# Optimization experiments

Hardware: AMD Instinct MI355X
Metric: run time of the kernel (lower is better)

Reference implementation:

```python
import jax, jax.numpy as jnp
import numpy as np
from jax import lax

N = 40       # num_users
K = 20       # num_channels
F = 3        # num_features (conv length dim)
SS = K * N   # state_size = 800
B = 16384


def _conv1d(x, w, b):
    # x: [B, C_in, L], w: [C_out, C_in, 3], SAME padding (pad=1)
    y = lax.conv_general_dilated(x, w, window_strides=(1,), padding=[(1, 1)],
                                 dimension_numbers=('NCH', 'OIH', 'NCH'))
    return y + b[None, :, None]


def _get_mask(state):
    # state: [B, SS, F]; status feature is index 2 (== -1 since F=3)
    visited = state[:, :, 2] != 0.0                      # [B, SS]
    vm = visited.reshape(B, K, N)                        # [B, K, N] (flat idx = chan*N + user)
    user_any = vm.any(axis=1)                            # [B, N]: user visited on any channel
    chan_full = vm.sum(axis=2) >= 2                      # [B, K]: channel has >=2 users
    mask = visited \
        | jnp.broadcast_to(user_any[:, None, :], (B, K, N)).reshape(B, SS) \
        | jnp.broadcast_to(chan_full[:, :, None], (B, K, N)).reshape(B, SS)
    return mask


def setup_inputs() -> dict:
    key = jax.random.key(0)
    ks = jax.random.split(key, 12)
    state = jax.random.normal(ks[0], (B, SS, F), jnp.float32)
    keep = jax.random.bernoulli(ks[1], 0.02, (B, SS)).astype(jnp.float32)
    state = state.at[:, :, 2].multiply(keep)
    s = 0.02
    w1 = jax.random.normal(ks[2], (128, SS, 3), jnp.float32) * s
    b1 = jnp.zeros((128,), jnp.float32)
    w2 = jax.random.normal(ks[3], (256, 128, 3), jnp.float32) * s
    b2 = jnp.zeros((256,), jnp.float32)
    w3 = jax.random.normal(ks[4], (128, 256, 3), jnp.float32) * s
    b3 = jnp.zeros((128,), jnp.float32)
    wl1 = jax.random.normal(ks[5], (64 * F, 128 * F), jnp.float32) * s   # [192, 384]
    bl1 = jnp.zeros((64 * F,), jnp.float32)
    wl2 = jax.random.normal(ks[6], (SS, 64 * F), jnp.float32) * s        # [800, 192]
    bl2 = jnp.zeros((SS,), jnp.float32)
    return {"state": state, "w1": w1, "b1": b1, "w2": w2, "b2": b2,
            "w3": w3, "b3": b3, "wl1": wl1, "bl1": bl1, "wl2": wl2, "bl2": bl2}


def reference(state, w1, b1, w2, b2, w3, b3, wl1, bl1, wl2, bl2):
    mask = _get_mask(state)
    x = jax.nn.relu(_conv1d(state, w1, b1))   # [B,128,3]
    x = jax.nn.relu(_conv1d(x, w2, b2))       # [B,256,3]
    x = jax.nn.relu(_conv1d(x, w3, b3))       # [B,128,3]
    x = x.reshape(B, -1)                      # [B,384]
    x = jax.nn.relu(x @ wl1.T + bl1)          # [B,192]
    out = x @ wl2.T + bl2                     # [B,800]
    return jnp.where(mask, -jnp.inf, out)
```

## Files before the change

kernel.cpp:

```cpp
#include <hip/hip_runtime.h>
#include <cstdint>
#include <cstddef>
#include <math.h>

typedef short bf16x8 __attribute__((ext_vector_type(8)));
typedef float f32x4 __attribute__((ext_vector_type(4)));
typedef unsigned long long u64;

#define NEG_HUGE (-3.0e38f)

__device__ __forceinline__ ushort f2bf(float x) {
    union { float f; uint32_t u; } a; a.f = x;
    uint32_t r = a.u + 0x7FFF + ((a.u >> 16) & 1);
    return (ushort)(r >> 16);
}

__global__ void prep_conv_T(const float* __restrict__ w, ushort* __restrict__ WT,
                            int Cin, int Cout, int Nrows, int Kpad) {
    int idx = blockIdx.x * 256 + threadIdx.x;
    if (idx >= Nrows * Kpad) return;
    int n = idx / Kpad, k = idx - n * Kpad;
    float val = 0.f;
    if (k < Cin * 3) {
        int co = n / 3, l = n % 3, ci = k / 3, lx = k % 3;
        int t = lx - l + 1;
        if (t >= 0 && t < 3) val = w[(co * Cin + ci) * 3 + t];
    }
    WT[idx] = f2bf(val);
}

__global__ void prep_lin_T(const float* __restrict__ wl, ushort* __restrict__ WT,
                           int K, int Nreal, int Npad) {
    int idx = blockIdx.x * 256 + threadIdx.x;
    if (idx >= Npad * K) return;
    int n = idx / K, k = idx - n * K;
    WT[idx] = (n < Nreal) ? f2bf(wl[n * K + k]) : (ushort)0;
}

#define SPB 64
#define LDS_X1   0
#define LDS_X2   49152
#define LDS_MASK 147456
#define LDS_TOTAL 153856

template<int NF, int MF, int KSTEPS, int LDX>
__device__ __forceinline__ void layer_mfma(const char* xlds,
                                           const ushort* __restrict__ WT, int ldw,
                                           int wn0, int mbase, int lane,
                                           f32x4 (&acc)[NF][MF]) {
    const int ml = lane & 15, kq = lane >> 4;
    #pragma unroll 4
    for (int ks = 0; ks < KSTEPS; ++ks) {
        bf16x8 af[NF];
        #pragma unroll
        for (int f = 0; f < NF; ++f)
            af[f] = *(const bf16x8*)(WT + (size_t)(wn0 + f * 16 + ml) * ldw + ks * 32 + kq * 8);
        bf16x8 bv[MF];
        #pragma unroll
        for (int mi = 0; mi < MF; ++mi) {
            int m = mbase + mi * 16 + ml;
            bv[mi] = *(const bf16x8*)(xlds + m * LDX + ((((ks * 4 + kq) * 16)) ^ ((m & 7) << 4)));
        }
        #pragma unroll
        for (int f = 0; f < NF; ++f)
            #pragma unroll
            for (int mi = 0; mi < MF; ++mi)
                acc[f][mi] = __builtin_amdgcn_mfma_f32_16x16x32_bf16(af[f], bv[mi], acc[f][mi], 0, 0, 0);
    }
}

template<int NF, int MF, bool RELU, bool BDIV3>
__device__ __forceinline__ void epi_lds(f32x4 (&acc)[NF][MF], char* xout, int ldo,
                                        const float* __restrict__ bias,
                                        int wn0, int mbase, int lane) {
    const int ml = lane & 15, nq4 = (lane >> 4) * 4;
    #pragma unroll
    for (int f = 0; f < NF; ++f) {
        const int n4 = wn0 + f * 16 + nq4;
        float bv[4];
        #pragma unroll
        for (int r = 0; r < 4; ++r) bv[r] = bias[BDIV3 ? (n4 + r) / 3 : (n4 + r)];
        #pragma unroll
        for (int mi = 0; mi < MF; ++mi) {
            int m = mbase + mi * 16 + ml;
            ushort4 o;
            float x0 = acc[f][mi][0] + bv[0];
            float x1 = acc[f][mi][1] + bv[1];
            float x2 = acc[f][mi][2] + bv[2];
            float x3 = acc[f][mi][3] + bv[3];
            if (RELU) { x0 = fmaxf(x0, 0.f); x1 = fmaxf(x1, 0.f);
                        x2 = fmaxf(x2, 0.f); x3 = fmaxf(x3, 0.f); }
            o.x = f2bf(x0); o.y = f2bf(x1); o.z = f2bf(x2); o.w = f2bf(x3);
            *(ushort4*)(xout + m * ldo + ((n4 * 2) ^ ((m & 7) << 4))) = o;
        }
    }
}

__global__ __launch_bounds__(512, 2)
void fused_net(const float* __restrict__ state,
               const ushort* __restrict__ W1T, const float* __restrict__ b1,
               const ushort* __restrict__ W2T, const float* __restrict__ b2,
               const ushort* __restrict__ W3T, const float* __restrict__ b3,
               const ushort* __restrict__ WL1T, const float* __restrict__ bl1,
               const ushort* __restrict__ WL2T, const float* __restrict__ bl2,
               float* __restrict__ out)
{
    extern __shared__ char lds[];
    const int tid = threadIdx.x;
    const int lane = tid & 63, wid = tid >> 6;
    const int m0 = blockIdx.x * SPB;
    uint32_t* maskw = (uint32_t*)(lds + LDS_MASK);
    char* stg = lds + LDS_X2;

    for (int i = tid; i < SPB * 25; i += 512) maskw[i] = 0;

    const int sr = tid >> 3, seg = tid & 7;
    const float* srow = state + (size_t)(m0 + sr) * 2400 + seg * 16;
    const int wn1 = wid * 48;

    f32x4 acc1[3][4];
    #pragma unroll
    for (int f = 0; f < 3; ++f)
        #pragma unroll
        for (int mi = 0; mi < 4; ++mi) acc1[f][mi] = (f32x4){0.f, 0.f, 0.f, 0.f};

    float4 svA[4], svB[4];
    auto loadc = [&](float4 (&sv)[4], int c) {
        int kb = c * 128 + seg * 16;
        if (kb <= 2384) {
            #pragma unroll
            for (int q = 0; q < 4; ++q) sv[q] = *(const float4*)(srow + c * 128 + q * 4);
        } else {
            #pragma unroll
            for (int q = 0; q < 4; ++q) sv[q] = (float4){0.f, 0.f, 0.f, 0.f};
        }
    };
    auto stage_write = [&](float4 (&sv)[4], int c) {
        int kbase = c * 128 + seg * 16;
        float fv[16] = {sv[0].x, sv[0].y, sv[0].z, sv[0].w,
                        sv[1].x, sv[1].y, sv[1].z, sv[1].w,
                        sv[2].x, sv[2].y, sv[2].z, sv[2].w,
                        sv[3].x, sv[3].y, sv[3].z, sv[3].w};
        bf16x8 h0, h1;
        #pragma unroll
        for (int j = 0; j < 8; ++j) h0[j] = (short)f2bf(fv[j]);
        #pragma unroll
        for (int j = 0; j < 8; ++j) h1[j] = (short)f2bf(fv[8 + j]);
        const int rb = sr * 256, xo = (sr & 7) << 4;
        *(bf16x8*)(stg + rb + ((seg * 32) ^ xo)) = h0;
        *(bf16x8*)(stg + rb + ((seg * 32 + 16) ^ xo)) = h1;
        int kmod = kbase % 3;
        uint32_t* mrow = maskw + sr * 25;
        #define MCHK(J) { if (fv[J] != 0.0f) { int a = (kbase + (J)) / 3; \
                          atomicOr(&mrow[a >> 5], 1u << (a & 31)); } }
        if (kmod == 0)      { MCHK(2) MCHK(5) MCHK(8) MCHK(11) MCHK(14) }
        else if (kmod == 1) { MCHK(1) MCHK(4) MCHK(7) MCHK(10) MCHK(13) }
        else                { MCHK(0) MCHK(3) MCHK(6) MCHK(9) MCHK(12) MCHK(15) }
        #undef MCHK
    };

    loadc(svA, 0);
    loadc(svB, 1);
    __syncthreads();

    #define C1STEP(SV, C, CN) \
        stage_write(SV, C); \
        __syncthreads(); \
        if ((CN) <= 18) loadc(SV, CN); \
        layer_mfma<3, 4, 4, 256>(stg, W1T + (C) * 128, 2432, wn1, 0, lane, acc1); \
        __syncthreads();

    for (int p = 0; p < 9; ++p) {
        int c0 = 2 * p;
        C1STEP(svA, c0, c0 + 2)
        C1STEP(svB, c0 + 1, c0 + 3)
    }
    C1STEP(svA, 18, 99)
    #undef C1STEP

    epi_lds<3, 4, true, true>(acc1, lds + LDS_X1, 768, b1, wn1, 0, lane);

    if (tid < SPB) {
        uint32_t* mw = maskw + tid * 25;
        const u64 M40 = (1ull << 40) - 1;
        u64 ua = 0; uint32_t cf = 0;
        #pragma unroll
        for (int g = 0; g < 5; ++g) {
            uint32_t w0 = mw[5*g], w1 = mw[5*g+1], w2 = mw[5*g+2], w3 = mw[5*g+3], w4 = mw[5*g+4];
            u64 c0 = ( (u64)w0        | ((u64)w1 << 32)) & M40;
            u64 c1 = (((u64)w1 >> 8)  | ((u64)w2 << 24)) & M40;
            u64 c2 = (((u64)w2 >> 16) | ((u64)w3 << 16)) & M40;
            u64 c3 = (((u64)w3 >> 24) | ((u64)w4 << 8))  & M40;
            ua |= c0 | c1 | c2 | c3;
            if (__popcll(c0) >= 2) cf |= 1u << (4*g);
            if (__popcll(c1) >= 2) cf |= 1u << (4*g+1);
            if (__popcll(c2) >= 2) cf |= 1u << (4*g+2);
            if (__popcll(c3) >= 2) cf |= 1u << (4*g+3);
        }
        #pragma unroll
        for (int g = 0; g < 5; ++g) {
            uint32_t w0 = mw[5*g], w1 = mw[5*g+1], w2 = mw[5*g+2], w3 = mw[5*g+3], w4 = mw[5*g+4];
            u64 c0 = ( (u64)w0        | ((u64)w1 << 32)) & M40;
            u64 c1 = (((u64)w1 >> 8)  | ((u64)w2 << 24)) & M40;
            u64 c2 = (((u64)w2 >> 16) | ((u64)w3 << 16)) & M40;
            u64 c3 = (((u64)w3 >> 24) | ((u64)w4 << 8))  & M40;
            u64 m0v = c0 | ua | (((cf >> (4*g))     & 1u) ? M40 : 0ull);
            u64 m1v = c1 | ua | (((cf >> (4*g + 1)) & 1u) ? M40 : 0ull);
            u64 m2v = c2 | ua | (((cf >> (4*g + 2)) & 1u) ? M40 : 0ull);
            u64 m3v = c3 | ua | (((cf >> (4*g + 3)) & 1u) ? M40 : 0ull);
            mw[5*g]   = (uint32_t)m0v;
            mw[5*g+1] = (uint32_t)(m0v >> 32) | (uint32_t)(m1v << 8);
            mw[5*g+2] = (uint32_t)(m1v >> 24) | (uint32_t)(m2v << 16);
            mw[5*g+3] = (uint32_t)(m2v >> 16) | (uint32_t)(m3v << 24);
            mw[5*g+4] = (uint32_t)(m3v >> 8);
        }
    }
    __syncthreads();

    f32x4 acc2[6][4];
    #pragma unroll
    for (int f = 0; f < 6; ++f)
        #pragma unroll
        for (int mi = 0; mi < 4; ++mi) acc2[f][mi] = (f32x4){0.f, 0.f, 0.f, 0.f};
    layer_mfma<6, 4, 12, 768>(lds + LDS_X1, W2T, 384, wid * 96, 0, lane, acc2);
    epi_lds<6, 4, true, true>(acc2, lds + LDS_X2, 1536, b2, wid * 96, 0, lane);
    __syncthreads();

    f32x4 acc3[3][4];
    #pragma unroll
    for (int f = 0; f < 3; ++f)
        #pragma unroll
        for (int mi = 0; mi < 4; ++mi) acc3[f][mi] = (f32x4){0.f, 0.f, 0.f, 0.f};
    layer_mfma<3, 4, 24, 1536>(lds + LDS_X2, W3T, 768, wid * 48, 0, lane, acc3);
    epi_lds<3, 4, true, true>(acc3, lds + LDS_X1, 768, b3, wid * 48, 0, lane);
    __syncthreads();

    const int mh = wid >> 2, nq = wid & 3;
    f32x4 acc4[3][2];
    #pragma unroll
    for (int f = 0; f < 3; ++f)
        #pragma unroll
        for (int mi = 0; mi < 2; ++mi) acc4[f][mi] = (f32x4){0.f, 0.f, 0.f, 0.f};
    layer_mfma<3, 2, 12, 768>(lds + LDS_X1, WL1T, 384, nq * 48, mh * 32, lane, acc4);
    epi_lds<3, 2, true, false>(acc4, lds + LDS_X2, 384, bl1, nq * 48, mh * 32, lane);
    __syncthreads();

    f32x4 acc5[7][4];
    #pragma unroll
    for (int f = 0; f < 7; ++f)
        #pragma unroll
        for (int mi = 0; mi < 4; ++mi) acc5[f][mi] = (f32x4){0.f, 0.f, 0.f, 0.f};
    layer_mfma<7, 4, 6, 384>(lds + LDS_X2, WL2T, 192, wid * 112, 0, lane, acc5);
    {
        const int ml = lane & 15, nq4 = (lane >> 4) * 4;
        #pragma unroll
        for (int f = 0; f < 7; ++f) {
            int nf = wid * 112 + f * 16;
            if (nf < 800) {
                int n4 = nf + nq4, sh = n4 & 31;
                float bv0 = bl2[n4], bv1 = bl2[n4 + 1], bv2 = bl2[n4 + 2], bv3 = bl2[n4 + 3];
                #pragma unroll
                for (int mi = 0; mi < 4; ++mi) {
                    int m = mi * 16 + ml;
                    uint32_t mwv = maskw[m * 25 + (nf >> 5)];
                    float4 v;
                    v.x = ((mwv >> (sh + 0)) & 1u) ? NEG_HUGE : (acc5[f][mi][0] + bv0);
                    v.y = ((mwv >> (sh + 1)) & 1u) ? NEG_HUGE : (acc5[f][mi][1] + bv1);
                    v.z = ((mwv >> (sh + 2)) & 1u) ? NEG_HUGE : (acc5[f][mi][2] + bv2);
                    v.w = ((mwv >> (sh + 3)) & 1u) ? NEG_HUGE : (acc5[f][mi][3] + bv3);
                    *(float4*)(out + (size_t)(m0 + m) * 800 + n4) = v;
                }
            }
        }
    }
}

__global__ void ws_fail_kernel(float* out) {
    if (threadIdx.x == 0 && blockIdx.x == 0) out[0] = NAN;
}

extern "C" void kernel_launch(void* const* d_in, const int* in_sizes, int n_in,
                              void* d_out, int out_size, void* d_ws, size_t ws_size,
                              hipStream_t stream) {
    const float* state = (const float*)d_in[0];
    const float* w1  = (const float*)d_in[1];
    const float* b1  = (const float*)d_in[2];
    const float* w2  = (const float*)d_in[3];
    const float* b2  = (const float*)d_in[4];
    const float* w3  = (const float*)d_in[5];
    const float* b3  = (const float*)d_in[6];
    const float* wl1 = (const float*)d_in[7];
    const float* bl1 = (const float*)d_in[8];
    const float* wl2 = (const float*)d_in[9];
    const float* bl2 = (const float*)d_in[10];
    float* out = (float*)d_out;

    char* ws = (char*)d_ws;
    size_t off = 0;
    auto carve = [&](size_t bytes) {
        char* p = ws + off;
        off = (off + bytes + 255) & ~(size_t)255;
        return p;
    };
    ushort* W1T  = (ushort*)carve(384ull * 2432 * 2);
    ushort* W2T  = (ushort*)carve(768ull * 384 * 2);
    ushort* W3T  = (ushort*)carve(384ull * 768 * 2);
    ushort* WL1T = (ushort*)carve(192ull * 384 * 2);
    ushort* WL2T = (ushort*)carve(896ull * 192 * 2);

    if (off > ws_size) {
        ws_fail_kernel<<<1, 64, 0, stream>>>(out);
        return;
    }

    prep_conv_T<<<(384 * 2432 + 255) / 256, 256, 0, stream>>>(w1, W1T, 800, 128, 384, 2432);
    prep_conv_T<<<(768 * 384 + 255) / 256, 256, 0, stream>>>(w2, W2T, 128, 256, 768, 384);
    prep_conv_T<<<(384 * 768 + 255) / 256, 256, 0, stream>>>(w3, W3T, 256, 128, 384, 768);
    prep_lin_T<<<(192 * 384 + 255) / 256, 256, 0, stream>>>(wl1, WL1T, 384, 192, 192);
    prep_lin_T<<<(896 * 192 + 255) / 256, 256, 0, stream>>>(wl2, WL2T, 192, 800, 896);

    hipFuncSetAttribute(reinterpret_cast<const void*>(fused_net),
                        hipFuncAttributeMaxDynamicSharedMemorySize, LDS_TOTAL);
    fused_net<<<256, 512, LDS_TOTAL, stream>>>(state, W1T, b1, W2T, b2, W3T, b3,
                                               WL1T, bl1, WL2T, bl2, out);
}
```

Baseline: 165.5 us.

## Split fused network into conv1 and rest kernels with smaller per-block tiles

Splits the single fused kernel into two. conv1_kernel streams the state, builds the mask and writes X1 and the mask to global workspace. rest_kernel loads X1 into LDS through global_load_lds and runs the remaining layers with software-prefetched weight fragments. Blocks now cover 32 samples instead of 64, which doubles the grid to 512 blocks, lowers LDS per block and improves CU occupancy on 256 CUs. The cost is an extra round-trip of X1 and the mask through global memory, one more kernel launch, and less weight reuse per block.

```diff
diff --git a/kernel.cpp b/kernel.cpp
--- a/kernel.cpp
+++ b/kernel.cpp
@@ -14,6 +14,15 @@
     uint32_t r = a.u + 0x7FFF + ((a.u >> 16) & 1);
     return (ushort)(r >> 16);
 }
+
+__device__ __forceinline__ void gload_lds16(const void* g, void* l) {
+    __builtin_amdgcn_global_load_lds(
+        (const __attribute__((address_space(1))) uint32_t*)g,
+        (__attribute__((address_space(3))) uint32_t*)l, 16, 0, 0);
+}
+
+#define WAITB() do { asm volatile("s_waitcnt lgkmcnt(0)" ::: "memory"); \
+    __builtin_amdgcn_sched_barrier(0); __builtin_amdgcn_s_barrier(); } while (0)
 
 __global__ void prep_conv_T(const float* __restrict__ w, ushort* __restrict__ WT,
                             int Cin, int Cout, int Nrows, int Kpad) {
@@ -37,151 +46,122 @@
     WT[idx] = (n < Nreal) ? f2bf(wl[n * K + k]) : (ushort)0;
 }
 
-#define SPB 64
-#define LDS_X1   0
-#define LDS_X2   49152
-#define LDS_MASK 147456
-#define LDS_TOTAL 153856
-
-template<int NF, int MF, int KSTEPS, int LDX>
-__device__ __forceinline__ void layer_mfma(const char* xlds,
-                                           const ushort* __restrict__ WT, int ldw,
-                                           int wn0, int mbase, int lane,
-                                           f32x4 (&acc)[NF][MF]) {
-    const int ml = lane & 15, kq = lane >> 4;
-    #pragma unroll 4
-    for (int ks = 0; ks < KSTEPS; ++ks) {
-        bf16x8 af[NF];
-        #pragma unroll
-        for (int f = 0; f < NF; ++f)
-            af[f] = *(const bf16x8*)(WT + (size_t)(wn0 + f * 16 + ml) * ldw + ks * 32 + kq * 8);
-        bf16x8 bv[MF];
-        #pragma unroll
-        for (int mi = 0; mi < MF; ++mi) {
-            int m = mbase + mi * 16 + ml;
-            bv[mi] = *(const bf16x8*)(xlds + m * LDX + ((((ks * 4 + kq) * 16)) ^ ((m & 7) << 4)));
-        }
-        #pragma unroll
-        for (int f = 0; f < NF; ++f)
-            #pragma unroll
-            for (int mi = 0; mi < MF; ++mi)
-                acc[f][mi] = __builtin_amdgcn_mfma_f32_16x16x32_bf16(af[f], bv[mi], acc[f][mi], 0, 0, 0);
-    }
-}
-
-template<int NF, int MF, bool RELU, bool BDIV3>
-__device__ __forceinline__ void epi_lds(f32x4 (&acc)[NF][MF], char* xout, int ldo,
-                                        const float* __restrict__ bias,
-                                        int wn0, int mbase, int lane) {
-    const int ml = lane & 15, nq4 = (lane >> 4) * 4;
-    #pragma unroll
-    for (int f = 0; f < NF; ++f) {
-        const int n4 = wn0 + f * 16 + nq4;
-        float bv[4];
-        #pragma unroll
-        for (int r = 0; r < 4; ++r) bv[r] = bias[BDIV3 ? (n4 + r) / 3 : (n4 + r)];
-        #pragma unroll
-        for (int mi = 0; mi < MF; ++mi) {
-            int m = mbase + mi * 16 + ml;
-            ushort4 o;
-            float x0 = acc[f][mi][0] + bv[0];
-            float x1 = acc[f][mi][1] + bv[1];
-            float x2 = acc[f][mi][2] + bv[2];
-            float x3 = acc[f][mi][3] + bv[3];
-            if (RELU) { x0 = fmaxf(x0, 0.f); x1 = fmaxf(x1, 0.f);
-                        x2 = fmaxf(x2, 0.f); x3 = fmaxf(x3, 0.f); }
-            o.x = f2bf(x0); o.y = f2bf(x1); o.z = f2bf(x2); o.w = f2bf(x3);
-            *(ushort4*)(xout + m * ldo + ((n4 * 2) ^ ((m & 7) << 4))) = o;
-        }
-    }
-}
-
 __global__ __launch_bounds__(512, 2)
-void fused_net(const float* __restrict__ state,
-               const ushort* __restrict__ W1T, const float* __restrict__ b1,
-               const ushort* __restrict__ W2T, const float* __restrict__ b2,
-               const ushort* __restrict__ W3T, const float* __restrict__ b3,
-               const ushort* __restrict__ WL1T, const float* __restrict__ bl1,
-               const ushort* __restrict__ WL2T, const float* __restrict__ bl2,
-               float* __restrict__ out)
+void conv1_kernel(const float* __restrict__ state, const ushort* __restrict__ W1T,
+                  const float* __restrict__ b1, ushort* __restrict__ X1g,
+                  uint32_t* __restrict__ maskg)
 {
-    extern __shared__ char lds[];
+    __shared__ ushort stg[2][32][128];
+    __shared__ uint32_t maskw[32][25];
     const int tid = threadIdx.x;
     const int lane = tid & 63, wid = tid >> 6;
-    const int m0 = blockIdx.x * SPB;
-    uint32_t* maskw = (uint32_t*)(lds + LDS_MASK);
-    char* stg = lds + LDS_X2;
-
-    for (int i = tid; i < SPB * 25; i += 512) maskw[i] = 0;
-
-    const int sr = tid >> 3, seg = tid & 7;
-    const float* srow = state + (size_t)(m0 + sr) * 2400 + seg * 16;
-    const int wn1 = wid * 48;
-
-    f32x4 acc1[3][4];
+    const int m0 = blockIdx.x * 32;
+
+    for (int i = tid; i < 800; i += 512) ((uint32_t*)maskw)[i] = 0;
+
+    const int sr = tid >> 4, seg = tid & 15;
+    const float* srow = state + (size_t)(m0 + sr) * 2400 + seg * 8;
+
+    f32x4 acc[3][2];
     #pragma unroll
     for (int f = 0; f < 3; ++f)
         #pragma unroll
-        for (int mi = 0; mi < 4; ++mi) acc1[f][mi] = (f32x4){0.f, 0.f, 0.f, 0.f};
-
-    float4 svA[4], svB[4];
-    auto loadc = [&](float4 (&sv)[4], int c) {
-        int kb = c * 128 + seg * 16;
-        if (kb <= 2384) {
-            #pragma unroll
-            for (int q = 0; q < 4; ++q) sv[q] = *(const float4*)(srow + c * 128 + q * 4);
+        for (int mi = 0; mi < 2; ++mi) acc[f][mi] = (f32x4){0.f, 0.f, 0.f, 0.f};
+
+    float4 svA[2], svB[2];
+    auto loadc = [&](float4 (&sv)[2], int c) {
+        int kb = c * 128 + seg * 8;
+        if (kb < 2400) {
+            sv[0] = *(const float4*)(srow + c * 128);
+            sv[1] = *(const float4*)(srow + c * 128 + 4);
         } else {
-            #pragma unroll
-            for (int q = 0; q < 4; ++q) sv[q] = (float4){0.f, 0.f, 0.f, 0.f};
+            sv[0] = (float4){0.f, 0.f, 0.f, 0.f};
+            sv[1] = (float4){0.f, 0.f, 0.f, 0.f};
         }
     };
-    auto stage_write = [&](float4 (&sv)[4], int c) {
-        int kbase = c * 128 + seg * 16;
-        float fv[16] = {sv[0].x, sv[0].y, sv[0].z, sv[0].w,
-                        sv[1].x, sv[1].y, sv[1].z, sv[1].w,
-                        sv[2].x, sv[2].y, sv[2].z, sv[2].w,
-                        sv[3].x, sv[3].y, sv[3].z, sv[3].w};
-        bf16x8 h0, h1;
-        #pragma unroll
-        for (int j = 0; j < 8; ++j) h0[j] = (short)f2bf(fv[j]);
-        #pragma unroll
-        for (int j = 0; j < 8; ++j) h1[j] = (short)f2bf(fv[8 + j]);
-        const int rb = sr * 256, xo = (sr & 7) << 4;
-        *(bf16x8*)(stg + rb + ((seg * 32) ^ xo)) = h0;
-        *(bf16x8*)(stg + rb + ((seg * 32 + 16) ^ xo)) = h1;
-        int kmod = kbase % 3;
-        uint32_t* mrow = maskw + sr * 25;
-        #define MCHK(J) { if (fv[J] != 0.0f) { int a = (kbase + (J)) / 3; \
-                          atomicOr(&mrow[a >> 5], 1u << (a & 31)); } }
-        if (kmod == 0)      { MCHK(2) MCHK(5) MCHK(8) MCHK(11) MCHK(14) }
-        else if (kmod == 1) { MCHK(1) MCHK(4) MCHK(7) MCHK(10) MCHK(13) }
-        else                { MCHK(0) MCHK(3) MCHK(6) MCHK(9) MCHK(12) MCHK(15) }
-        #undef MCHK
+    auto stage_write = [&](float4 (&sv)[2], int c, int buf) {
+        int kbase = c * 128 + seg * 8;
+        float fv[8] = {sv[0].x, sv[0].y, sv[0].z, sv[0].w,
+                       sv[1].x, sv[1].y, sv[1].z, sv[1].w};
+        bf16x8 h;
+        #pragma unroll
+        for (int j = 0; j < 8; ++j) h[j] = (short)f2bf(fv[j]);
+        *(bf16x8*)((char*)&stg[buf][sr][0] + ((seg * 16) ^ ((sr & 7) << 4))) = h;
+        #pragma unroll
+        for (int j = 0; j < 8; ++j) {
+            int k = kbase + j;
+            if (k % 3 == 2 && fv[j] != 0.0f) {
+                int a = k / 3;
+                atomicOr(&maskw[sr][a >> 5], 1u << (a & 31));
+            }
+        }
+    };
+    auto layer1 = [&](int buf, const ushort* WT) {
+        const int ml = lane & 15, kq = lane >> 4;
+        const ushort* wrow = WT + (size_t)(wid * 48 + ml) * 2432 + kq * 8;
+        #pragma unroll
+        for (int ks = 0; ks < 4; ++ks) {
+            bf16x8 af[3];
+            #pragma unroll
+            for (int f = 0; f < 3; ++f)
+                af[f] = *(const bf16x8*)(wrow + (size_t)f * 16 * 2432 + ks * 32);
+            bf16x8 bv[2];
+            #pragma unroll
+            for (int mi = 0; mi < 2; ++mi) {
+                int m = mi * 16 + ml;
+                bv[mi] = *(const bf16x8*)((const char*)&stg[buf][0][0] + m * 256 +
+                                          (((ks * 4 + kq) * 16) ^ ((m & 7) << 4)));
+            }
+            #pragma unroll
+            for (int f = 0; f < 3; ++f)
+                #pragma unroll
+                for (int mi = 0; mi < 2; ++mi)
+                    acc[f][mi] = __builtin_amdgcn_mfma_f32_16x16x32_bf16(af[f], bv[mi], acc[f][mi], 0, 0, 0);
+        }
     };
 
     loadc(svA, 0);
     loadc(svB, 1);
     __syncthreads();
 
-    #define C1STEP(SV, C, CN) \
-        stage_write(SV, C); \
-        __syncthreads(); \
-        if ((CN) <= 18) loadc(SV, CN); \
-        layer_mfma<3, 4, 4, 256>(stg, W1T + (C) * 128, 2432, wn1, 0, lane, acc1); \
-        __syncthreads();
-
+    #pragma unroll 1
     for (int p = 0; p < 9; ++p) {
-        int c0 = 2 * p;
-        C1STEP(svA, c0, c0 + 2)
-        C1STEP(svB, c0 + 1, c0 + 3)
-    }
-    C1STEP(svA, 18, 99)
-    #undef C1STEP
-
-    epi_lds<3, 4, true, true>(acc1, lds + LDS_X1, 768, b1, wn1, 0, lane);
-
-    if (tid < SPB) {
-        uint32_t* mw = maskw + tid * 25;
+        int c0 = 2 * p, c1 = 2 * p + 1;
+        stage_write(svA, c0, 0);
+        WAITB();
+        loadc(svA, c0 + 2);
+        layer1(0, W1T + c0 * 128);
+        stage_write(svB, c1, 1);
+        WAITB();
+        loadc(svB, c1 + 2);
+        layer1(1, W1T + c1 * 128);
+    }
+    stage_write(svA, 18, 0);
+    WAITB();
+    layer1(0, W1T + 18 * 128);
+
+    {
+        const int ml = lane & 15, nq4 = (lane >> 4) * 4;
+        #pragma unroll
+        for (int f = 0; f < 3; ++f) {
+            int n4 = wid * 48 + f * 16 + nq4;
+            float bv0 = b1[n4 / 3], bv1 = b1[(n4 + 1) / 3];
+            float bv2 = b1[(n4 + 2) / 3], bv3 = b1[(n4 + 3) / 3];
+            #pragma unroll
+            for (int mi = 0; mi < 2; ++mi) {
+                int m = mi * 16 + ml;
+                ushort4 o;
+                o.x = f2bf(fmaxf(acc[f][mi][0] + bv0, 0.f));
+                o.y = f2bf(fmaxf(acc[f][mi][1] + bv1, 0.f));
+                o.z = f2bf(fmaxf(acc[f][mi][2] + bv2, 0.f));
+                o.w = f2bf(fmaxf(acc[f][mi][3] + bv3, 0.f));
+                *(ushort4*)(X1g + (size_t)(m0 + m) * 384 + n4) = o;
+            }
+        }
+    }
+
+    if (tid < 32) {
+        uint32_t* mw = &maskw[tid][0];
         const u64 M40 = (1ull << 40) - 1;
         u64 ua = 0; uint32_t cf = 0;
         #pragma unroll
@@ -197,6 +177,7 @@
             if (__popcll(c2) >= 2) cf |= 1u << (4*g+2);
             if (__popcll(c3) >= 2) cf |= 1u << (4*g+3);
         }
+        uint32_t* mg = maskg + (size_t)(m0 + tid) * 25;
         #pragma unroll
         for (int g = 0; g < 5; ++g) {
             uint32_t w0 = mw[5*g], w1 = mw[5*g+1], w2 = mw[5*g+2], w3 = mw[5*g+3], w4 = mw[5*g+4];
@@ -208,49 +189,137 @@
             u64 m1v = c1 | ua | (((cf >> (4*g + 1)) & 1u) ? M40 : 0ull);
             u64 m2v = c2 | ua | (((cf >> (4*g + 2)) & 1u) ? M40 : 0ull);
             u64 m3v = c3 | ua | (((cf >> (4*g + 3)) & 1u) ? M40 : 0ull);
-            mw[5*g]   = (uint32_t)m0v;
-            mw[5*g+1] = (uint32_t)(m0v >> 32) | (uint32_t)(m1v << 8);
-            mw[5*g+2] = (uint32_t)(m1v >> 24) | (uint32_t)(m2v << 16);
-            mw[5*g+3] = (uint32_t)(m2v >> 16) | (uint32_t)(m3v << 24);
-            mw[5*g+4] = (uint32_t)(m3v >> 8);
-        }
-    }
-    __syncthreads();
-
-    f32x4 acc2[6][4];
+            mg[5*g]   = (uint32_t)m0v;
+            mg[5*g+1] = (uint32_t)(m0v >> 32) | (uint32_t)(m1v << 8);
+            mg[5*g+2] = (uint32_t)(m1v >> 24) | (uint32_t)(m2v << 16);
+            mg[5*g+3] = (uint32_t)(m2v >> 16) | (uint32_t)(m3v << 24);
+            mg[5*g+4] = (uint32_t)(m3v >> 8);
+        }
+    }
+}
+
+template<int NF, int MF, int KPAIRS, int LDX>
+__device__ __forceinline__ void layer_pf(const char* xlds, const ushort* __restrict__ WT,
+                                         const int ldw, int wn0, int mbase, int lane,
+                                         f32x4 (&acc)[NF][MF]) {
+    const int ml = lane & 15, kq = lane >> 4;
+    const ushort* wrow = WT + (size_t)(wn0 + ml) * ldw + kq * 8;
+    bf16x8 afA[NF], afB[NF];
+    #pragma unroll
+    for (int f = 0; f < NF; ++f) afA[f] = *(const bf16x8*)(wrow + (size_t)f * 16 * ldw);
+    #pragma unroll
+    for (int p = 0; p < KPAIRS; ++p) {
+        const int ks0 = 2 * p, ks1 = 2 * p + 1;
+        #pragma unroll
+        for (int f = 0; f < NF; ++f)
+            afB[f] = *(const bf16x8*)(wrow + (size_t)f * 16 * ldw + ks1 * 32);
+        bf16x8 bv[MF];
+        #pragma unroll
+        for (int mi = 0; mi < MF; ++mi) {
+            int m = mbase + mi * 16 + ml;
+            bv[mi] = *(const bf16x8*)(xlds + m * LDX + (((ks0 * 4 + kq) * 16) ^ ((m & 7) << 4)));
+        }
+        #pragma unroll
+        for (int f = 0; f < NF; ++f)
+            #pragma unroll
+            for (int mi = 0; mi < MF; ++mi)
+                acc[f][mi] = __builtin_amdgcn_mfma_f32_16x16x32_bf16(afA[f], bv[mi], acc[f][mi], 0, 0, 0);
+        const int ksn = (p + 1 < KPAIRS) ? (2 * p + 2) : 0;
+        #pragma unroll
+        for (int f = 0; f < NF; ++f)
+            afA[f] = *(const bf16x8*)(wrow + (size_t)f * 16 * ldw + ksn * 32);
+        #pragma unroll
+        for (int mi = 0; mi < MF; ++mi) {
+            int m = mbase + mi * 16 + ml;
+            bv[mi] = *(const bf16x8*)(xlds + m * LDX + (((ks1 * 4 + kq) * 16) ^ ((m & 7) << 4)));
+        }
+        #pragma unroll
+        for (int f = 0; f < NF; ++f)
+            #pragma unroll
+            for (int mi = 0; mi < MF; ++mi)
+                acc[f][mi] = __builtin_amdgcn_mfma_f32_16x16x32_bf16(afB[f], bv[mi], acc[f][mi], 0, 0, 0);
+    }
+}
+
+template<int NF, int MF, bool RELU, bool BDIV3>
+__device__ __forceinline__ void epi_lds(f32x4 (&acc)[NF][MF], char* xout, int ldo,
+                                        const float* __restrict__ bias,
+                                        int wn0, int mbase, int lane) {
+    const int ml = lane & 15, nq4 = (lane >> 4) * 4;
+    #pragma unroll
+    for (int f = 0; f < NF; ++f) {
+        const int n4 = wn0 + f * 16 + nq4;
+        float bv[4];
+        #pragma unroll
+        for (int r = 0; r < 4; ++r) bv[r] = bias[BDIV3 ? (n4 + r) / 3 : (n4 + r)];
+        #pragma unroll
+        for (int mi = 0; mi < MF; ++mi) {
+            int m = mbase + mi * 16 + ml;
+            float x0 = acc[f][mi][0] + bv[0], x1 = acc[f][mi][1] + bv[1];
+            float x2 = acc[f][mi][2] + bv[2], x3 = acc[f][mi][3] + bv[3];
+            if (RELU) { x0 = fmaxf(x0, 0.f); x1 = fmaxf(x1, 0.f);
+                        x2 = fmaxf(x2, 0.f); x3 = fmaxf(x3, 0.f); }
+            ushort4 o = {f2bf(x0), f2bf(x1), f2bf(x2), f2bf(x3)};
+            *(ushort4*)(xout + m * ldo + ((n4 * 2) ^ ((m & 7) << 4))) = o;
+        }
+    }
+}
+
+__global__ __launch_bounds__(512, 2)
+void rest_kernel(const ushort* __restrict__ X1g,
+                 const ushort* __restrict__ W2T, const float* __restrict__ b2,
+                 const ushort* __restrict__ W3T, const float* __restrict__ b3,
+                 const ushort* __restrict__ WL1T, const float* __restrict__ bl1,
+                 const ushort* __restrict__ WL2T, const float* __restrict__ bl2,
+                 const uint32_t* __restrict__ maskg, float* __restrict__ out)
+{
+    extern __shared__ char lds[];
+    char* X1L = lds;
+    char* X2L = lds + 24576;
+    const int tid = threadIdx.x, lane = tid & 63, wid = tid >> 6;
+    const int m0 = blockIdx.x * 32;
+
+    #pragma unroll
+    for (int i = 0; i < 3; ++i) {
+        int s = i * 512 + tid;
+        int row = s / 48, o = s - row * 48;
+        int go = (o & ~7) | ((o & 7) ^ (row & 7));
+        gload_lds16(X1g + (size_t)(m0 + row) * 384 + go * 8, X1L + s * 16);
+    }
+    __syncthreads();
+
+    f32x4 acc2[6][2];
     #pragma unroll
     for (int f = 0; f < 6; ++f)
         #pragma unroll
-        for (int mi = 0; mi < 4; ++mi) acc2[f][mi] = (f32x4){0.f, 0.f, 0.f, 0.f};
-    layer_mfma<6, 4, 12, 768>(lds + LDS_X1, W2T, 384, wid * 96, 0, lane, acc2);
-    epi_lds<6, 4, true, true>(acc2, lds + LDS_X2, 1536, b2, wid * 96, 0, lane);
-    __syncthreads();
-
-    f32x4 acc3[3][4];
+        for (int mi = 0; mi < 2; ++mi) acc2[f][mi] = (f32x4){0.f, 0.f, 0.f, 0.f};
+    layer_pf<6, 2, 6, 768>(X1L, W2T, 384, wid * 96, 0, lane, acc2);
+    epi_lds<6, 2, true, true>(acc2, X2L, 1536, b2, wid * 96, 0, lane);
+    __syncthreads();
+
+    f32x4 acc3[3][2];
     #pragma unroll
     for (int f = 0; f < 3; ++f)
         #pragma unroll
-        for (int mi = 0; mi < 4; ++mi) acc3[f][mi] = (f32x4){0.f, 0.f, 0.f, 0.f};
-    layer_mfma<3, 4, 24, 1536>(lds + LDS_X2, W3T, 768, wid * 48, 0, lane, acc3);
-    epi_lds<3, 4, true, true>(acc3, lds + LDS_X1, 768, b3, wid * 48, 0, lane);
+        for (int mi = 0; mi < 2; ++mi) acc3[f][mi] = (f32x4){0.f, 0.f, 0.f, 0.f};
+    layer_pf<3, 2, 12, 1536>(X2L, W3T, 768, wid * 48, 0, lane, acc3);
+    epi_lds<3, 2, true, true>(acc3, X1L, 768, b3, wid * 48, 0, lane);
     __syncthreads();
 
     const int mh = wid >> 2, nq = wid & 3;
-    f32x4 acc4[3][2];
-    #pragma unroll
-    for (int f = 0; f < 3; ++f)
-        #pragma unroll
-        for (int mi = 0; mi < 2; ++mi) acc4[f][mi] = (f32x4){0.f, 0.f, 0.f, 0.f};
-    layer_mfma<3, 2, 12, 768>(lds + LDS_X1, WL1T, 384, nq * 48, mh * 32, lane, acc4);
-    epi_lds<3, 2, true, false>(acc4, lds + LDS_X2, 384, bl1, nq * 48, mh * 32, lane);
-    __syncthreads();
-
-    f32x4 acc5[7][4];
+    f32x4 acc4[3][1];
+    #pragma unroll
+    for (int f = 0; f < 3; ++f) acc4[f][0] = (f32x4){0.f, 0.f, 0.f, 0.f};
+    layer_pf<3, 1, 6, 768>(X1L, WL1T, 384, nq * 48, mh * 16, lane, acc4);
+    epi_lds<3, 1, true, false>(acc4, X2L, 384, bl1, nq * 48, mh * 16, lane);
+    __syncthreads();
+
+    f32x4 acc5[7][2];
     #pragma unroll
     for (int f = 0; f < 7; ++f)
         #pragma unroll
-        for (int mi = 0; mi < 4; ++mi) acc5[f][mi] = (f32x4){0.f, 0.f, 0.f, 0.f};
-    layer_mfma<7, 4, 6, 384>(lds + LDS_X2, WL2T, 192, wid * 112, 0, lane, acc5);
+        for (int mi = 0; mi < 2; ++mi) acc5[f][mi] = (f32x4){0.f, 0.f, 0.f, 0.f};
+    layer_pf<7, 2, 3, 384>(X2L, WL2T, 192, wid * 112, 0, lane, acc5);
     {
         const int ml = lane & 15, nq4 = (lane >> 4) * 4;
         #pragma unroll
@@ -260,9 +329,9 @@
                 int n4 = nf + nq4, sh = n4 & 31;
                 float bv0 = bl2[n4], bv1 = bl2[n4 + 1], bv2 = bl2[n4 + 2], bv3 = bl2[n4 + 3];
                 #pragma unroll
-                for (int mi = 0; mi < 4; ++mi) {
+                for (int mi = 0; mi < 2; ++mi) {
                     int m = mi * 16 + ml;
-                    uint32_t mwv = maskw[m * 25 + (nf >> 5)];
+                    uint32_t mwv = maskg[(size_t)(m0 + m) * 25 + (nf >> 5)];
                     float4 v;
                     v.x = ((mwv >> (sh + 0)) & 1u) ? NEG_HUGE : (acc5[f][mi][0] + bv0);
                     v.y = ((mwv >> (sh + 1)) & 1u) ? NEG_HUGE : (acc5[f][mi][1] + bv1);
@@ -307,6 +376,8 @@
     ushort* W3T  = (ushort*)carve(384ull * 768 * 2);
     ushort* WL1T = (ushort*)carve(192ull * 384 * 2);
     ushort* WL2T = (ushort*)carve(896ull * 192 * 2);
+    ushort* X1g  = (ushort*)carve(16384ull * 384 * 2);
+    uint32_t* maskg = (uint32_t*)carve(16384ull * 25 * 4);
 
     if (off > ws_size) {
         ws_fail_kernel<<<1, 64, 0, stream>>>(out);
@@ -319,8 +390,10 @@
     prep_lin_T<<<(192 * 384 + 255) / 256, 256, 0, stream>>>(wl1, WL1T, 384, 192, 192);
     prep_lin_T<<<(896 * 192 + 255) / 256, 256, 0, stream>>>(wl2, WL2T, 192, 800, 896);
 
-    hipFuncSetAttribute(reinterpret_cast<const void*>(fused_net),
-                        hipFuncAttributeMaxDynamicSharedMemorySize, LDS_TOTAL);
-    fused_net<<<256, 512, LDS_TOTAL, stream>>>(state, W1T, b1, W2T, b2, W3T, b3,
-                                               WL1T, bl1, WL2T, bl2, out);
-}
+    conv1_kernel<<<512, 512, 0, stream>>>(state, W1T, b1, X1g, maskg);
+
+    hipFuncSetAttribute(reinterpret_cast<const void*>(rest_kernel),
+                        hipFuncAttributeMaxDynamicSharedMemorySize, 73728);
+    rest_kernel<<<512, 512, 73728, stream>>>(X1g, W2T, b2, W3T, b3,
+                                             WL1T, bl1, WL2T, bl2, maskg, out);
+}
```

Result: slower. 252.0 us (+52.3%).
